# Optimization experiments

Measured on AMD Instinct MI355X. Metric: run time of the kernel, lower is better.

## Reference

```python
import jax, jax.numpy as jnp
import numpy as np

SCALE = 32.0 / 16.0  # alpha / r

def setup_inputs() -> dict:
    key = jax.random.key(0)
    k1, k2, k3, k4, k5 = jax.random.split(key, 5)
    B, S, D_in, D_out, R = 4, 4096, 4096, 4096, 16
    x = jax.random.normal(k1, (B, S, D_in), dtype=jnp.float32)
    W = jax.random.normal(k2, (D_out, D_in), dtype=jnp.float32) * 0.02
    b = jax.random.normal(k3, (D_out,), dtype=jnp.float32) * 0.02
    lora_A = jax.random.normal(k4, (D_in, R), dtype=jnp.float32) * 0.01
    lora_B = jax.random.normal(k5, (R, D_out), dtype=jnp.float32) * 0.01
    return {"x": x, "W": W, "b": b, "lora_A": lora_A, "lora_B": lora_B}

def reference(x, W, b, lora_A, lora_B):
    # base: x @ W.T + b  (nn.Linear semantics: weight is [out_f, in_f])
    out = jnp.einsum("bsd,od->bso", x, W) + b
    # LoRA path: (x @ A) @ B, scaled residual add
    lora = jnp.einsum("bsr,ro->bso", jnp.einsum("bsd,dr->bsr", x, lora_A), lora_B)
    return out + SCALE * lora
```

## Files before the change

kernel.cpp:

```cpp
#include <hip/hip_runtime.h>
#include <hip/hip_bf16.h>

typedef __bf16 bf16_t;
typedef __bf16 bf16x8 __attribute__((ext_vector_type(8)));
typedef __bf16 bf16x4 __attribute__((ext_vector_type(4)));
typedef float floatx4 __attribute__((ext_vector_type(4)));

#define M_DIM 16384
#define N_DIM 4096
#define K_DIM 4096
#define R_DIM 16
#define LORA_SCALE 2.0f

__device__ __forceinline__ void async_copy16(void* lds, const void* gptr) {
  __builtin_amdgcn_global_load_lds(
      (__attribute__((address_space(1))) void*)(gptr),
      (__attribute__((address_space(3))) void*)(lds),
      16, 0, 0);
}

__global__ void cvt_kernel(const float* __restrict__ src,
                           bf16_t* __restrict__ dst, int n8) {
  const int idx = blockIdx.x * blockDim.x + threadIdx.x;
  if (idx >= n8) return;
  const float4 a = ((const float4*)src)[idx * 2 + 0];
  const float4 b = ((const float4*)src)[idx * 2 + 1];
  bf16x8 v;
  v[0] = (bf16_t)a.x; v[1] = (bf16_t)a.y; v[2] = (bf16_t)a.z; v[3] = (bf16_t)a.w;
  v[4] = (bf16_t)b.x; v[5] = (bf16_t)b.y; v[6] = (bf16_t)b.z; v[7] = (bf16_t)b.w;
  ((bf16x8*)dst)[idx] = v;
}

__launch_bounds__(256, 2)
__global__ void lora_xa_bf16(const bf16_t* __restrict__ X,
                             const float* __restrict__ A,
                             bf16_t* __restrict__ T) {
  __shared__ bf16_t Xs[64 * 64];
  __shared__ bf16_t At[16 * 64];
  const int tid  = threadIdx.x;
  const int wave = tid >> 6;
  const int lane = tid & 63;
  const int quad = lane >> 4;
  const int l15  = lane & 15;
  const int gm0  = blockIdx.x * 64;

  floatx4 acc = {0.f, 0.f, 0.f, 0.f};
  for (int k0 = 0; k0 < K_DIM; k0 += 64) {
#pragma unroll
    for (int j = 0; j < 2; ++j) {
      const int i   = wave * 2 + j;
      const int row = i * 8 + (lane >> 3);
      const int col = (lane & 7) * 8;
      async_copy16(&Xs[i * 512], X + (size_t)(gm0 + row) * K_DIM + k0 + col);
    }
    {
      const int c  = tid >> 4;
      const int k4 = (tid & 15) * 4;
#pragma unroll
      for (int j = 0; j < 4; ++j)
        At[c * 64 + k4 + j] = (bf16_t)A[(size_t)(k0 + k4 + j) * R_DIM + c];
    }
    __syncthreads();
#pragma unroll
    for (int h = 0; h < 2; ++h) {
      const int kk = h * 32;
      const bf16x8 a = *(const bf16x8*)&Xs[(wave * 16 + l15) * 64 + kk + quad * 8];
      const bf16x8 b = *(const bf16x8*)&At[l15 * 64 + kk + quad * 8];
      acc = __builtin_amdgcn_mfma_f32_16x16x32_bf16(a, b, acc, 0, 0, 0);
    }
    __syncthreads();
  }
#pragma unroll
  for (int r = 0; r < 4; ++r) {
    const int row = gm0 + wave * 16 + quad * 4 + r;
    T[(size_t)row * R_DIM + l15] = (bf16_t)(LORA_SCALE * acc[r]);
  }
}

__launch_bounds__(256, 2)
__global__ void lora_xa_f32(const float* __restrict__ X,
                            const float* __restrict__ A,
                            bf16_t* __restrict__ T) {
  __shared__ bf16_t Xs[64 * 64];
  __shared__ bf16_t At[16 * 64];
  const int tid  = threadIdx.x;
  const int wave = tid >> 6;
  const int lane = tid & 63;
  const int quad = lane >> 4;
  const int l15  = lane & 15;
  const int gm0  = blockIdx.x * 64;

  floatx4 acc = {0.f, 0.f, 0.f, 0.f};
  for (int k0 = 0; k0 < K_DIM; k0 += 64) {
#pragma unroll
    for (int i = 0; i < 4; ++i) {
      const int idx  = tid + i * 256;
      const int row  = idx >> 4;
      const int colf = idx & 15;
      const float4 v = *(const float4*)&X[(size_t)(gm0 + row) * K_DIM + k0 + colf * 4];
      bf16x4 w;
      w[0] = (bf16_t)v.x; w[1] = (bf16_t)v.y; w[2] = (bf16_t)v.z; w[3] = (bf16_t)v.w;
      *(bf16x4*)&Xs[row * 64 + colf * 4] = w;
    }
    {
      const int c  = tid >> 4;
      const int k4 = (tid & 15) * 4;
#pragma unroll
      for (int j = 0; j < 4; ++j)
        At[c * 64 + k4 + j] = (bf16_t)A[(size_t)(k0 + k4 + j) * R_DIM + c];
    }
    __syncthreads();
#pragma unroll
    for (int h = 0; h < 2; ++h) {
      const int kk = h * 32;
      const bf16x8 a = *(const bf16x8*)&Xs[(wave * 16 + l15) * 64 + kk + quad * 8];
      const bf16x8 b = *(const bf16x8*)&At[l15 * 64 + kk + quad * 8];
      acc = __builtin_amdgcn_mfma_f32_16x16x32_bf16(a, b, acc, 0, 0, 0);
    }
    __syncthreads();
  }
#pragma unroll
  for (int r = 0; r < 4; ++r) {
    const int row = gm0 + wave * 16 + quad * 4 + r;
    T[(size_t)row * R_DIM + l15] = (bf16_t)(LORA_SCALE * acc[r]);
  }
}

__launch_bounds__(256, 2)
__global__ void main_bf16(const bf16_t* __restrict__ X,
                          const bf16_t* __restrict__ W,
                          const float* __restrict__ bias,
                          const float* __restrict__ loraB,
                          const bf16_t* __restrict__ T,
                          float* __restrict__ out) {
  __shared__ bf16_t As[128 * 32];
  __shared__ bf16_t Bs[128 * 32];
  const int tid  = threadIdx.x;
  const int wave = tid >> 6;
  const int lane = tid & 63;
  const int quad = lane >> 4;
  const int l15  = lane & 15;
  const int gm   = (blockIdx.x >> 5) * 128;
  const int gn   = (blockIdx.x & 31) * 128;
  const int wr   = wave >> 1;
  const int wc   = wave & 1;

  floatx4 acc[4][4];
#pragma unroll
  for (int i = 0; i < 4; ++i)
#pragma unroll
    for (int j = 0; j < 4; ++j) acc[i][j] = (floatx4){0.f, 0.f, 0.f, 0.f};

  const int st_sub = lane >> 2;
  const int st_col = (lane & 3) * 8;

  for (int k0 = 0; k0 < K_DIM; k0 += 32) {
#pragma unroll
    for (int j = 0; j < 2; ++j) {
      const int i   = wave * 2 + j;
      const int row = i * 16 + st_sub;
      async_copy16(&As[i * 512], X + (size_t)(gm + row) * K_DIM + k0 + st_col);
      async_copy16(&Bs[i * 512], W + (size_t)(gn + row) * K_DIM + k0 + st_col);
    }
    __syncthreads();
    bf16x8 a_frag[4], b_frag[4];
#pragma unroll
    for (int im = 0; im < 4; ++im)
      a_frag[im] = *(const bf16x8*)&As[(wr * 64 + im * 16 + l15) * 32 + quad * 8];
#pragma unroll
    for (int in = 0; in < 4; ++in)
      b_frag[in] = *(const bf16x8*)&Bs[(wc * 64 + in * 16 + l15) * 32 + quad * 8];
#pragma unroll
    for (int im = 0; im < 4; ++im)
#pragma unroll
      for (int in = 0; in < 4; ++in)
        acc[im][in] = __builtin_amdgcn_mfma_f32_16x16x32_bf16(
            a_frag[im], b_frag[in], acc[im][in], 0, 0, 0);
    __syncthreads();
  }

  if (tid < 128) {
    const int row = tid;
    const bf16_t* tp = T + (size_t)(gm + row) * R_DIM;
    *(uint4*)&As[row * 32]      = *(const uint4*)tp;
    *(uint4*)&As[row * 32 + 8]  = *(const uint4*)(tp + 8);
    *(uint4*)&As[row * 32 + 16] = make_uint4(0, 0, 0, 0);
    *(uint4*)&As[row * 32 + 24] = make_uint4(0, 0, 0, 0);
  } else {
    const int n = tid - 128;
#pragma unroll
    for (int r = 0; r < R_DIM; ++r)
      Bs[n * 32 + r] = (bf16_t)loraB[(size_t)r * N_DIM + gn + n];
    *(uint4*)&Bs[n * 32 + 16] = make_uint4(0, 0, 0, 0);
    *(uint4*)&Bs[n * 32 + 24] = make_uint4(0, 0, 0, 0);
  }
  __syncthreads();
  {
    bf16x8 a_frag[4], b_frag[4];
#pragma unroll
    for (int im = 0; im < 4; ++im)
      a_frag[im] = *(const bf16x8*)&As[(wr * 64 + im * 16 + l15) * 32 + quad * 8];
#pragma unroll
    for (int in = 0; in < 4; ++in)
      b_frag[in] = *(const bf16x8*)&Bs[(wc * 64 + in * 16 + l15) * 32 + quad * 8];
#pragma unroll
    for (int im = 0; im < 4; ++im)
#pragma unroll
      for (int in = 0; in < 4; ++in)
        acc[im][in] = __builtin_amdgcn_mfma_f32_16x16x32_bf16(
            a_frag[im], b_frag[in], acc[im][in], 0, 0, 0);
  }

#pragma unroll
  for (int in = 0; in < 4; ++in) {
    const int col = gn + wc * 64 + in * 16 + l15;
    const float bv = bias[col];
#pragma unroll
    for (int im = 0; im < 4; ++im) {
      const int row0 = gm + wr * 64 + im * 16 + quad * 4;
#pragma unroll
      for (int r = 0; r < 4; ++r)
        out[(size_t)(row0 + r) * N_DIM + col] = acc[im][in][r] + bv;
    }
  }
}

__launch_bounds__(256, 2)
__global__ void main_f32(const float* __restrict__ X,
                         const float* __restrict__ W,
                         const float* __restrict__ bias,
                         const float* __restrict__ loraB,
                         const bf16_t* __restrict__ T,
                         float* __restrict__ out) {
  __shared__ bf16_t As[128 * 32];
  __shared__ bf16_t Bs[128 * 32];
  const int tid  = threadIdx.x;
  const int wave = tid >> 6;
  const int lane = tid & 63;
  const int quad = lane >> 4;
  const int l15  = lane & 15;
  const int gm   = (blockIdx.x >> 5) * 128;
  const int gn   = (blockIdx.x & 31) * 128;
  const int wr   = wave >> 1;
  const int wc   = wave & 1;

  floatx4 acc[4][4];
#pragma unroll
  for (int i = 0; i < 4; ++i)
#pragma unroll
    for (int j = 0; j < 4; ++j) acc[i][j] = (floatx4){0.f, 0.f, 0.f, 0.f};

  for (int k0 = 0; k0 < K_DIM; k0 += 32) {
#pragma unroll
    for (int i = 0; i < 4; ++i) {
      const int idx  = tid + i * 256;
      const int row  = idx >> 3;
      const int colf = idx & 7;
      const float4 va = *(const float4*)&X[(size_t)(gm + row) * K_DIM + k0 + colf * 4];
      const float4 vb = *(const float4*)&W[(size_t)(gn + row) * K_DIM + k0 + colf * 4];
      bf16x4 wa, wb;
      wa[0] = (bf16_t)va.x; wa[1] = (bf16_t)va.y; wa[2] = (bf16_t)va.z; wa[3] = (bf16_t)va.w;
      wb[0] = (bf16_t)vb.x; wb[1] = (bf16_t)vb.y; wb[2] = (bf16_t)vb.z; wb[3] = (bf16_t)vb.w;
      *(bf16x4*)&As[row * 32 + colf * 4] = wa;
      *(bf16x4*)&Bs[row * 32 + colf * 4] = wb;
    }
    __syncthreads();
    bf16x8 a_frag[4], b_frag[4];
#pragma unroll
    for (int im = 0; im < 4; ++im)
      a_frag[im] = *(const bf16x8*)&As[(wr * 64 + im * 16 + l15) * 32 + quad * 8];
#pragma unroll
    for (int in = 0; in < 4; ++in)
      b_frag[in] = *(const bf16x8*)&Bs[(wc * 64 + in * 16 + l15) * 32 + quad * 8];
#pragma unroll
    for (int im = 0; im < 4; ++im)
#pragma unroll
      for (int in = 0; in < 4; ++in)
        acc[im][in] = __builtin_amdgcn_mfma_f32_16x16x32_bf16(
            a_frag[im], b_frag[in], acc[im][in], 0, 0, 0);
    __syncthreads();
  }

  if (tid < 128) {
    const int row = tid;
    const bf16_t* tp = T + (size_t)(gm + row) * R_DIM;
    *(uint4*)&As[row * 32]      = *(const uint4*)tp;
    *(uint4*)&As[row * 32 + 8]  = *(const uint4*)(tp + 8);
    *(uint4*)&As[row * 32 + 16] = make_uint4(0, 0, 0, 0);
    *(uint4*)&As[row * 32 + 24] = make_uint4(0, 0, 0, 0);
  } else {
    const int n = tid - 128;
#pragma unroll
    for (int r = 0; r < R_DIM; ++r)
      Bs[n * 32 + r] = (bf16_t)loraB[(size_t)r * N_DIM + gn + n];
    *(uint4*)&Bs[n * 32 + 16] = make_uint4(0, 0, 0, 0);
    *(uint4*)&Bs[n * 32 + 24] = make_uint4(0, 0, 0, 0);
  }
  __syncthreads();
  {
    bf16x8 a_frag[4], b_frag[4];
#pragma unroll
    for (int im = 0; im < 4; ++im)
      a_frag[im] = *(const bf16x8*)&As[(wr * 64 + im * 16 + l15) * 32 + quad * 8];
#pragma unroll
    for (int in = 0; in < 4; ++in)
      b_frag[in] = *(const bf16x8*)&Bs[(wc * 64 + in * 16 + l15) * 32 + quad * 8];
#pragma unroll
    for (int im = 0; im < 4; ++im)
#pragma unroll
      for (int in = 0; in < 4; ++in)
        acc[im][in] = __builtin_amdgcn_mfma_f32_16x16x32_bf16(
            a_frag[im], b_frag[in], acc[im][in], 0, 0, 0);
  }

#pragma unroll
  for (int in = 0; in < 4; ++in) {
    const int col = gn + wc * 64 + in * 16 + l15;
    const float bv = bias[col];
#pragma unroll
    for (int im = 0; im < 4; ++im) {
      const int row0 = gm + wr * 64 + im * 16 + quad * 4;
#pragma unroll
      for (int r = 0; r < 4; ++r)
        out[(size_t)(row0 + r) * N_DIM + col] = acc[im][in][r] + bv;
    }
  }
}

extern "C" void kernel_launch(void* const* d_in, const int* in_sizes, int n_in,
                              void* d_out, int out_size, void* d_ws, size_t ws_size,
                              hipStream_t stream) {
  const float* X    = (const float*)d_in[0];
  const float* W    = (const float*)d_in[1];
  const float* bias = (const float*)d_in[2];
  const float* lA   = (const float*)d_in[3];
  const float* lB   = (const float*)d_in[4];
  float* out = (float*)d_out;

  bf16_t* T = (bf16_t*)d_ws;
  const size_t offX = 512 * 1024;
  const size_t offW = offX + (size_t)M_DIM * K_DIM * sizeof(bf16_t);
  const size_t need = offW + (size_t)N_DIM * K_DIM * sizeof(bf16_t);

  if (ws_size >= need) {
    bf16_t* Xb = (bf16_t*)((char*)d_ws + offX);
    bf16_t* Wb = (bf16_t*)((char*)d_ws + offW);
    {
      const int n8 = M_DIM * K_DIM / 8;
      cvt_kernel<<<(n8 + 255) / 256, 256, 0, stream>>>(X, Xb, n8);
    }
    {
      const int n8 = N_DIM * K_DIM / 8;
      cvt_kernel<<<(n8 + 255) / 256, 256, 0, stream>>>(W, Wb, n8);
    }
    lora_xa_bf16<<<M_DIM / 64, 256, 0, stream>>>(Xb, lA, T);
    main_bf16<<<(M_DIM / 128) * (N_DIM / 128), 256, 0, stream>>>(
        Xb, Wb, bias, lB, T, out);
  } else {
    lora_xa_f32<<<M_DIM / 64, 256, 0, stream>>>(X, lA, T);
    main_f32<<<(M_DIM / 128) * (N_DIM / 128), 256, 0, stream>>>(
        X, W, bias, lB, T, out);
  }
}
```

Baseline: 1.140 ms.

## Replace bf16 GEMM with 256x256 8-wave double-buffered swizzled pipelined kernel

Replaces the 128x128, 4-wave, single-buffered main GEMM with a 256x256 tile, 8-wave kernel. It stages K=64 slices into 128KB of dynamic LDS with double buffering, an XOR-swizzled layout and interleaved async global-to-LDS loads. MFMA work is split into quarter phases separated by raw s_barrier, with setprio and explicit vmcnt waits so copies overlap compute. Blocks are remapped for L2 locality. This aims to cut global traffic per FLOP and hide load latency, at the cost of much higher register and LDS use, likely limiting occupancy to one block per CU.

```diff
diff --git a/kernel.cpp b/kernel.cpp
--- a/kernel.cpp
+++ b/kernel.cpp
@@ -17,6 +17,12 @@
       (__attribute__((address_space(1))) void*)(gptr),
       (__attribute__((address_space(3))) void*)(lds),
       16, 0, 0);
+}
+
+__device__ __forceinline__ void block_barrier() {
+  asm volatile("" ::: "memory");
+  __builtin_amdgcn_s_barrier();
+  asm volatile("" ::: "memory");
 }
 
 __global__ void cvt_kernel(const float* __restrict__ src,
@@ -126,60 +132,137 @@
   }
 }
 
-__launch_bounds__(256, 2)
-__global__ void main_bf16(const bf16_t* __restrict__ X,
-                          const bf16_t* __restrict__ W,
-                          const float* __restrict__ bias,
-                          const float* __restrict__ loraB,
-                          const bf16_t* __restrict__ T,
-                          float* __restrict__ out) {
-  __shared__ bf16_t As[128 * 32];
-  __shared__ bf16_t Bs[128 * 32];
+#define LD_A(AQ)                                                               \
+  _Pragma("unroll") for (int i_ = 0; i_ < 4; ++i_) {                           \
+    const int r_ = (rowA + ((AQ) * 4 + i_) * 16) * 64;                         \
+    af[i_][0] = *(const bf16x8*)&Ab[r_ + ((quad    ) ^ swz) * 8];              \
+    af[i_][1] = *(const bf16x8*)&Ab[r_ + ((quad + 4) ^ swz) * 8];              \
+  }
+
+#define LD_B(BQ)                                                               \
+  _Pragma("unroll") for (int j_ = 0; j_ < 2; ++j_) {                           \
+    const int r_ = (rowB + ((BQ) * 2 + j_) * 16) * 64;                         \
+    bfr[j_][0] = *(const bf16x8*)&Bb[r_ + ((quad    ) ^ swz) * 8];             \
+    bfr[j_][1] = *(const bf16x8*)&Bb[r_ + ((quad + 4) ^ swz) * 8];             \
+  }
+
+#define MFMA16(AQ, BQ)                                                         \
+  __builtin_amdgcn_s_setprio(1);                                               \
+  _Pragma("unroll") for (int i_ = 0; i_ < 4; ++i_)                             \
+  _Pragma("unroll") for (int j_ = 0; j_ < 2; ++j_) {                           \
+    acc[(AQ) * 4 + i_][(BQ) * 2 + j_] =                                        \
+        __builtin_amdgcn_mfma_f32_16x16x32_bf16(                               \
+            af[i_][0], bfr[j_][0], acc[(AQ) * 4 + i_][(BQ) * 2 + j_], 0, 0, 0);\
+    acc[(AQ) * 4 + i_][(BQ) * 2 + j_] =                                        \
+        __builtin_amdgcn_mfma_f32_16x16x32_bf16(                               \
+            af[i_][1], bfr[j_][1], acc[(AQ) * 4 + i_][(BQ) * 2 + j_], 0, 0, 0);\
+  }                                                                            \
+  __builtin_amdgcn_s_setprio(0);
+
+__launch_bounds__(512, 2)
+__global__ void main8_bf16(const bf16_t* __restrict__ X,
+                           const bf16_t* __restrict__ W,
+                           const float* __restrict__ bias,
+                           const float* __restrict__ loraB,
+                           const bf16_t* __restrict__ T,
+                           float* __restrict__ out) {
+  extern __shared__ bf16_t lds[];
+  bf16_t* As = lds;
+  bf16_t* Bs = lds + 32768;
+
   const int tid  = threadIdx.x;
   const int wave = tid >> 6;
   const int lane = tid & 63;
   const int quad = lane >> 4;
   const int l15  = lane & 15;
-  const int gm   = (blockIdx.x >> 5) * 128;
-  const int gn   = (blockIdx.x & 31) * 128;
-  const int wr   = wave >> 1;
-  const int wc   = wave & 1;
-
-  floatx4 acc[4][4];
-#pragma unroll
-  for (int i = 0; i < 4; ++i)
+  const int swz  = l15 & 7;
+  const int wr   = wave >> 2;
+  const int wc   = wave & 3;
+
+  const int b   = blockIdx.x;
+  const int swb = (b & 7) * 128 + (b >> 3);
+  const int gm  = (swb >> 4) * 256;
+  const int gn  = (swb & 15) * 256;
+
+  const int rowA = wr * 128 + l15;
+  const int rowB = wc * 64 + l15;
+
+  const int srow  = wave * 8 + (lane >> 3);
+  const int sslot = (lane & 7) ^ ((lane >> 3) & 7);
+  const bf16_t* gA = X + (size_t)(gm + srow) * K_DIM + sslot * 8;
+  const bf16_t* gB = W + (size_t)(gn + srow) * K_DIM + sslot * 8;
+
+  auto stageA = [&](int bsel, int u, int t) {
+    async_copy16(As + bsel * 16384 + u * 4096 + wave * 512,
+                 gA + (size_t)u * 64 * K_DIM + t * 64);
+  };
+  auto stageB = [&](int bsel, int u, int t) {
+    async_copy16(Bs + bsel * 16384 + u * 4096 + wave * 512,
+                 gB + (size_t)u * 64 * K_DIM + t * 64);
+  };
+
+  floatx4 acc[8][4];
+#pragma unroll
+  for (int i = 0; i < 8; ++i)
 #pragma unroll
     for (int j = 0; j < 4; ++j) acc[i][j] = (floatx4){0.f, 0.f, 0.f, 0.f};
 
-  const int st_sub = lane >> 2;
-  const int st_col = (lane & 3) * 8;
-
-  for (int k0 = 0; k0 < K_DIM; k0 += 32) {
-#pragma unroll
-    for (int j = 0; j < 2; ++j) {
-      const int i   = wave * 2 + j;
-      const int row = i * 16 + st_sub;
-      async_copy16(&As[i * 512], X + (size_t)(gm + row) * K_DIM + k0 + st_col);
-      async_copy16(&Bs[i * 512], W + (size_t)(gn + row) * K_DIM + k0 + st_col);
-    }
-    __syncthreads();
-    bf16x8 a_frag[4], b_frag[4];
-#pragma unroll
-    for (int im = 0; im < 4; ++im)
-      a_frag[im] = *(const bf16x8*)&As[(wr * 64 + im * 16 + l15) * 32 + quad * 8];
-#pragma unroll
-    for (int in = 0; in < 4; ++in)
-      b_frag[in] = *(const bf16x8*)&Bs[(wc * 64 + in * 16 + l15) * 32 + quad * 8];
-#pragma unroll
-    for (int im = 0; im < 4; ++im)
-#pragma unroll
-      for (int in = 0; in < 4; ++in)
-        acc[im][in] = __builtin_amdgcn_mfma_f32_16x16x32_bf16(
-            a_frag[im], b_frag[in], acc[im][in], 0, 0, 0);
-    __syncthreads();
-  }
-
-  if (tid < 128) {
+#pragma unroll
+  for (int u = 0; u < 4; ++u) stageA(0, u, 0);
+#pragma unroll
+  for (int u = 0; u < 4; ++u) stageB(0, u, 0);
+  stageA(1, 0, 1); stageA(1, 2, 1);
+  asm volatile("s_waitcnt vmcnt(2)" ::: "memory");
+  block_barrier();
+
+  const int NITER = K_DIM / 128;
+  for (int i = 0; i < NITER; ++i) {
+    const int t1 = 2 * i + 1, t2 = 2 * i + 2, t3 = 2 * i + 3;
+    const bool last = (i == NITER - 1);
+    bf16x8 af[4][2];
+    bf16x8 bfr[2][2];
+
+    {
+      const bf16_t* Ab = As;
+      const bf16_t* Bb = Bs;
+      LD_A(0); LD_B(0);
+      stageA(1, 1, t1); stageA(1, 3, t1);
+      stageB(1, 0, t1); stageB(1, 1, t1); stageB(1, 2, t1); stageB(1, 3, t1);
+      block_barrier(); MFMA16(0, 0); block_barrier();
+      LD_B(1);
+      block_barrier(); MFMA16(0, 1); block_barrier();
+      LD_A(1);
+      if (!last) { stageA(0, 0, t2); stageA(0, 2, t2); }
+      block_barrier(); MFMA16(1, 1); block_barrier();
+      LD_B(0);
+      block_barrier(); MFMA16(1, 0);
+      if (last) asm volatile("s_waitcnt vmcnt(0)" ::: "memory");
+      else      asm volatile("s_waitcnt vmcnt(2)" ::: "memory");
+      block_barrier();
+    }
+    {
+      const bf16_t* Ab = As + 16384;
+      const bf16_t* Bb = Bs + 16384;
+      LD_A(0); LD_B(0);
+      if (!last) {
+        stageA(0, 1, t2); stageA(0, 3, t2);
+        stageB(0, 0, t2); stageB(0, 1, t2); stageB(0, 2, t2); stageB(0, 3, t2);
+      }
+      block_barrier(); MFMA16(0, 0); block_barrier();
+      LD_B(1);
+      block_barrier(); MFMA16(0, 1); block_barrier();
+      LD_A(1);
+      if (!last) { stageA(1, 0, t3); stageA(1, 2, t3); }
+      block_barrier(); MFMA16(1, 1); block_barrier();
+      LD_B(0);
+      block_barrier(); MFMA16(1, 0);
+      if (last) asm volatile("s_waitcnt vmcnt(0)" ::: "memory");
+      else      asm volatile("s_waitcnt vmcnt(2)" ::: "memory");
+      block_barrier();
+    }
+  }
+
+  if (tid < 256) {
     const int row = tid;
     const bf16_t* tp = T + (size_t)(gm + row) * R_DIM;
     *(uint4*)&As[row * 32]      = *(const uint4*)tp;
@@ -187,7 +270,7 @@
     *(uint4*)&As[row * 32 + 16] = make_uint4(0, 0, 0, 0);
     *(uint4*)&As[row * 32 + 24] = make_uint4(0, 0, 0, 0);
   } else {
-    const int n = tid - 128;
+    const int n = tid - 256;
 #pragma unroll
     for (int r = 0; r < R_DIM; ++r)
       Bs[n * 32 + r] = (bf16_t)loraB[(size_t)r * N_DIM + gn + n];
@@ -196,19 +279,19 @@
   }
   __syncthreads();
   {
-    bf16x8 a_frag[4], b_frag[4];
-#pragma unroll
-    for (int im = 0; im < 4; ++im)
-      a_frag[im] = *(const bf16x8*)&As[(wr * 64 + im * 16 + l15) * 32 + quad * 8];
+    bf16x8 afr[8]; bf16x8 bft[4];
+#pragma unroll
+    for (int im = 0; im < 8; ++im)
+      afr[im] = *(const bf16x8*)&As[(wr * 128 + im * 16 + l15) * 32 + quad * 8];
 #pragma unroll
     for (int in = 0; in < 4; ++in)
-      b_frag[in] = *(const bf16x8*)&Bs[(wc * 64 + in * 16 + l15) * 32 + quad * 8];
-#pragma unroll
-    for (int im = 0; im < 4; ++im)
+      bft[in] = *(const bf16x8*)&Bs[(wc * 64 + in * 16 + l15) * 32 + quad * 8];
+#pragma unroll
+    for (int im = 0; im < 8; ++im)
 #pragma unroll
       for (int in = 0; in < 4; ++in)
         acc[im][in] = __builtin_amdgcn_mfma_f32_16x16x32_bf16(
-            a_frag[im], b_frag[in], acc[im][in], 0, 0, 0);
+            afr[im], bft[in], acc[im][in], 0, 0, 0);
   }
 
 #pragma unroll
@@ -216,8 +299,8 @@
     const int col = gn + wc * 64 + in * 16 + l15;
     const float bv = bias[col];
 #pragma unroll
-    for (int im = 0; im < 4; ++im) {
-      const int row0 = gm + wr * 64 + im * 16 + quad * 4;
+    for (int im = 0; im < 8; ++im) {
+      const int row0 = gm + wr * 128 + im * 16 + quad * 4;
 #pragma unroll
       for (int r = 0; r < 4; ++r)
         out[(size_t)(row0 + r) * N_DIM + col] = acc[im][in][r] + bv;
@@ -354,7 +437,14 @@
       cvt_kernel<<<(n8 + 255) / 256, 256, 0, stream>>>(W, Wb, n8);
     }
     lora_xa_bf16<<<M_DIM / 64, 256, 0, stream>>>(Xb, lA, T);
-    main_bf16<<<(M_DIM / 128) * (N_DIM / 128), 256, 0, stream>>>(
+    static bool attr_set = false;
+    if (!attr_set) {
+      (void)hipFuncSetAttribute(reinterpret_cast<const void*>(main8_bf16),
+                                hipFuncAttributeMaxDynamicSharedMemorySize,
+                                131072);
+      attr_set = true;
+    }
+    main8_bf16<<<(M_DIM / 256) * (N_DIM / 256), 512, 131072, stream>>>(
         Xb, Wb, bias, lB, T, out);
   } else {
     lora_xa_f32<<<M_DIM / 64, 256, 0, stream>>>(X, lA, T);
```

New measurement: 990.2 us. -13.2%, faster.
